# Performance work log

Hardware: AMD Instinct MI355X
Metric: run time of the kernel (lower is better)

Reference implementation:

```python
import jax, jax.numpy as jnp
import numpy as np

B, S, D, H = 4, 2048, 1024, 16
DK = D // H
THETA = 10000.0


def _rope(x, pos):
    # x: [..., s, d_k] interleaved-pair rotation (GPT-NeoX/torch-from-scratch style)
    half = DK // 2
    inv_freq = 1.0 / (THETA ** (jnp.arange(half, dtype=jnp.float32) * 2.0 / DK))
    ang = pos.astype(jnp.float32)[:, None] * inv_freq  # [s, half]
    cos, sin = jnp.cos(ang), jnp.sin(ang)
    x1, x2 = x[..., 0::2], x[..., 1::2]
    out = jnp.stack([x1 * cos - x2 * sin, x1 * sin + x2 * cos], axis=-1)
    return out.reshape(x.shape)


def setup_inputs() -> dict:
    key = jax.random.key(0)
    ks = jax.random.split(key, 5)
    w_scale = 1.0 / np.sqrt(D)
    return {
        "x": jax.random.normal(ks[0], (B, S, D), dtype=jnp.float32),
        "W_q": jax.random.normal(ks[1], (D, D), dtype=jnp.float32) * w_scale,
        "W_k": jax.random.normal(ks[2], (D, D), dtype=jnp.float32) * w_scale,
        "W_v": jax.random.normal(ks[3], (D, D), dtype=jnp.float32) * w_scale,
        "W_o": jax.random.normal(ks[4], (D, D), dtype=jnp.float32) * w_scale,
        "token_positions": jnp.arange(S, dtype=jnp.int32),
    }


def reference(x, W_q, W_k, W_v, W_o, token_positions):
    b, s, d = x.shape

    def proj(W):  # x @ W.T, split heads -> [b, h, s, d_k]
        y = jnp.einsum('bsd,ed->bse', x, W)
        return y.reshape(b, s, H, DK).transpose(0, 2, 1, 3)

    Q, K, V = proj(W_q), proj(W_k), proj(W_v)
    Q = _rope(Q, token_positions)
    K = _rope(K, token_positions)

    scores = jnp.einsum('bhqd,bhkd->bhqk', Q, K) / jnp.sqrt(jnp.float32(DK))
    causal = jnp.tril(jnp.ones((s, s), dtype=bool))
    scores = jnp.where(causal, scores, -jnp.inf)
    attn = jax.nn.softmax(scores, axis=-1)
    out = jnp.einsum('bhqk,bhkd->bhqd', attn, V)
    out = out.transpose(0, 2, 1, 3).reshape(b, s, d)
    return jnp.einsum('bsd,ed->bse', out, W_o)
```

## Files before the change

kernel.cpp:

```cpp
#include <hip/hip_runtime.h>
#include <stdint.h>

#define B_ 4
#define S_ 2048
#define D_ 1024
#define H_ 16
#define DK_ 64
#define M_ (B_*S_)

typedef __attribute__((ext_vector_type(8))) short short8;
typedef __attribute__((ext_vector_type(4))) float f32x4;
typedef __attribute__((ext_vector_type(16))) float f32x16;
typedef __attribute__((ext_vector_type(2))) unsigned int u32x2;

static __device__ __forceinline__ float bf2f(unsigned short s) {
  union { unsigned u; float f; } v; v.u = ((unsigned)s) << 16; return v.f;
}
static __device__ __forceinline__ unsigned short f2bf(float f) {
  union { float f; unsigned u; } v; v.f = f;
  unsigned r = v.u + 0x7fffu + ((v.u >> 16) & 1u);
  return (unsigned short)(r >> 16);
}
static __device__ __forceinline__ unsigned cvtpk_bf16(float lo, float hi) {
  unsigned r;
  asm("v_cvt_pk_bf16_f32 %0, %1, %2" : "=v"(r) : "v"(lo), "v"(hi));
  return r;
}

#define GLDS16(g, l) __builtin_amdgcn_global_load_lds( \
    (const __attribute__((address_space(1))) unsigned int*)(g), \
    (__attribute__((address_space(3))) unsigned int*)(l), 16, 0, 0)

__global__ void cvt_all_kernel(const float* __restrict__ x,
                               const float* __restrict__ w0, const float* __restrict__ w1,
                               const float* __restrict__ w2, const float* __restrict__ w3,
                               const int* __restrict__ pos,
                               unsigned short* __restrict__ xb,
                               unsigned short* __restrict__ o0, unsigned short* __restrict__ o1,
                               unsigned short* __restrict__ o2, unsigned short* __restrict__ o3,
                               float2* __restrict__ tab) {
  int idx = blockIdx.x * 256 + threadIdx.x;
  if (idx >= 3145728) {
    int tix = idx - 3145728;
    int s = tix >> 5, j = tix & 31;
    float freq = exp2f(-(float)j * (13.287712379549449f / 32.0f));
    float ang = (float)pos[s] * freq;
    float sn, cs;
    sincosf(ang, &sn, &cs);
    tab[tix] = make_float2(cs, sn);
    return;
  }
  const float* src; unsigned short* dst; int i;
  if (idx < 2097152) { src = x; dst = xb; i = idx; }
  else {
    int widx = idx - 2097152;
    int w = widx >> 18; i = widx & 262143;
    src = (w == 0) ? w0 : (w == 1) ? w1 : (w == 2) ? w2 : w3;
    dst = (w == 0) ? o0 : (w == 1) ? o1 : (w == 2) ? o2 : o3;
  }
  float4 v = ((const float4*)src)[i];
  ushort4 o;
  o.x = f2bf(v.x); o.y = f2bf(v.y); o.z = f2bf(v.z); o.w = f2bf(v.w);
  ((ushort4*)dst)[i] = o;
}

#define GEMM_BODY \
  __shared__ __align__(16) char lA[2][128*128]; \
  __shared__ __align__(16) char lB[2][128*128]; \
  int t = threadIdx.x; \
  int wave = t >> 6, lane = t & 63; \
  int ln15 = lane & 15, lgrp = lane >> 4; \
  int wr = wave >> 1, wc = wave & 1; \
  f32x4 acc[4][4]; \
  _Pragma("unroll") \
  for (int m = 0; m < 4; ++m) \
    _Pragma("unroll") \
    for (int n = 0; n < 4; ++n) { f32x4 z = {0.f,0.f,0.f,0.f}; acc[m][n] = z; } \
  const char* pA[4]; const char* pB[4]; int sdst[4]; \
  _Pragma("unroll") \
  for (int i_ = 0; i_ < 4; ++i_) { \
    int a_ = (i_*256 + t) << 4; \
    int r_ = a_ >> 7; \
    int cb_ = (a_ & 127) ^ ((r_ & 7) << 4); \
    sdst[i_] = a_; \
    pA[i_] = Ab + (size_t)r_*(K*2) + cb_; \
    pB[i_] = Bb + (size_t)r_*(K*2) + cb_; \
  } \
  GSTAGE(0); \
  __syncthreads(); \
  { int cur = 0; \
    for (int k0 = 0; k0 < K; k0 += 64) { \
      if (k0 + 64 < K) GSTAGE(cur ^ 1); \
      GEMM_COMPUTE(cur); \
      __syncthreads(); \
      cur ^= 1; \
    } }

#define GSTAGE(bufi) do { \
    _Pragma("unroll") \
    for (int i_ = 0; i_ < 4; ++i_) { \
      GLDS16(pA[i_], lA[bufi] + sdst[i_]); \
      GLDS16(pB[i_], lB[bufi] + sdst[i_]); \
      pA[i_] += 128; pB[i_] += 128; \
    } \
  } while (0)

#define GEMM_COMPUTE(bufi) do { \
    const char* cA_ = lA[bufi]; \
    const char* cB_ = lB[bufi]; \
    _Pragma("unroll") \
    for (int kf = 0; kf < 2; ++kf) { \
      int cb = kf*64 + lgrp*16; \
      short8 af[4], bfr[4]; \
      _Pragma("unroll") \
      for (int m = 0; m < 4; ++m) { \
        int r = wr*64 + m*16 + ln15; \
        af[m] = *(const short8*)(cA_ + r*128 + (cb ^ ((r & 7) << 4))); \
      } \
      _Pragma("unroll") \
      for (int n = 0; n < 4; ++n) { \
        int r = wc*64 + n*16 + ln15; \
        bfr[n] = *(const short8*)(cB_ + r*128 + (cb ^ ((r & 7) << 4))); \
      } \
      __builtin_amdgcn_s_setprio(1); \
      _Pragma("unroll") \
      for (int m = 0; m < 4; ++m) \
        _Pragma("unroll") \
        for (int n = 0; n < 4; ++n) \
          acc[m][n] = __builtin_amdgcn_mfma_f32_16x16x32_bf16(af[m], bfr[n], acc[m][n], 0, 0, 0); \
      __builtin_amdgcn_s_setprio(0); \
    } \
  } while (0)

__global__ __launch_bounds__(256) void gemm_qkv(const unsigned short* __restrict__ A,
                                                const unsigned short* __restrict__ W,
                                                const float2* __restrict__ Tab,
                                                unsigned short* __restrict__ Qo,
                                                unsigned short* __restrict__ Ko,
                                                unsigned short* __restrict__ Vo) {
  const int K = 1024;
  int bid = blockIdx.x;
  int wg = (bid & 7) * 192 + (bid >> 3);
  int bm = wg / 24, bn = wg % 24;
  const char* Ab = (const char*)A + (size_t)bm * 128 * (K*2);
  const char* Bb = (const char*)W + (size_t)bn * 128 * (K*2);
  GEMM_BODY

  if (bn < 16) {
    unsigned short* Out = (bn < 8) ? Qo : Ko;
    float qs = (bn < 8) ? (0.125f * 1.4426950408889634f) : 1.0f;
#pragma unroll
    for (int m = 0; m < 4; ++m)
#pragma unroll
      for (int n = 0; n < 4; ++n)
#pragma unroll
        for (int r = 0; r < 4; ++r) {
          int row = bm*128 + wr*64 + m*16 + lgrp*4 + r;
          int cc = (bn & 7)*128 + wc*64 + n*16 + ln15;
          int b = row >> 11, s = row & (S_-1);
          int h = cc >> 6, dk = cc & 63;
          float v = acc[m][n][r];
          float p = __shfl_xor(v, 1);
          float2 cssn = Tab[(s << 5) + (dk >> 1)];
          float sgn = (dk & 1) ? cssn.y : -cssn.y;
          float o = (v * cssn.x + p * sgn) * qs;
          Out[(((size_t)(b*H_ + h)*S_ + s) << 6) + dk] = f2bf(o);
        }
  } else {
#pragma unroll
    for (int m = 0; m < 4; ++m)
#pragma unroll
      for (int n = 0; n < 4; ++n)
#pragma unroll
        for (int r = 0; r < 4; ++r) {
          int row = bm*128 + wr*64 + m*16 + lgrp*4 + r;
          int cc = (bn - 16)*128 + wc*64 + n*16 + ln15;
          int b = row >> 11, s = row & (S_-1);
          int h = cc >> 6, dk = cc & 63;
          Vo[(((size_t)(b*H_ + h)*DK_ + dk) * S_) + s] = f2bf(acc[m][n][r]);
        }
  }
}

__global__ __launch_bounds__(256) void gemm_out(const unsigned short* __restrict__ A,
                                                const unsigned short* __restrict__ W,
                                                float* __restrict__ Out) {
  const int K = 1024, N = 1024;
  int bid = blockIdx.x;
  int wg = (bid & 7) * 64 + (bid >> 3);
  int bm = wg >> 3, bn = wg & 7;
  const char* Ab = (const char*)A + (size_t)bm * 128 * (K*2);
  const char* Bb = (const char*)W + (size_t)bn * 128 * (K*2);
  GEMM_BODY

#pragma unroll
  for (int m = 0; m < 4; ++m)
#pragma unroll
    for (int n = 0; n < 4; ++n)
#pragma unroll
      for (int r = 0; r < 4; ++r) {
        int row = bm*128 + wr*64 + m*16 + lgrp*4 + r;
        int col = bn*128 + wc*64 + n*16 + ln15;
        Out[(size_t)row * N + col] = acc[m][n][r];
      }
}

__global__ __launch_bounds__(512) void attn_kernel(const unsigned short* __restrict__ Q,
                                                   const unsigned short* __restrict__ Kg,
                                                   const unsigned short* __restrict__ VT,
                                                   unsigned short* __restrict__ O) {
  int bid = blockIdx.x;
  int bh = bid & 63;
  int grp = bid >> 6;
  int qt = (grp < 4) ? (7 - grp) : (grp - 4);
  int b = bh >> 4, h = bh & 15;
  const int qbase = qt * 256;
  const unsigned short* Qp = Q + (((size_t)bh * S_ + qbase) << 6);
  const char* Kp = (const char*)(Kg + ((size_t)bh * S_ << 6));
  const char* Vp = (const char*)(VT + (size_t)bh * DK_ * S_);

  __shared__ __align__(16) char lK[3][64*128];
  __shared__ __align__(16) char lV[3][64*128];

  int t = threadIdx.x, wave = t >> 6, lane = t & 63;
  int ln31 = lane & 31, hi = lane >> 5;
  int qw = wave * 32;
  int qg = qbase + qw + ln31;

  short8 qf[4];
#pragma unroll
  for (int kk = 0; kk < 4; ++kk)
    qf[kk] = *(const short8*)(Qp + (size_t)(qw + ln31)*64 + kk*16 + hi*8);

  f32x16 oc[2];
#pragma unroll
  for (int dh = 0; dh < 2; ++dh)
#pragma unroll
    for (int r = 0; r < 16; ++r) oc[dh][r] = 0.f;
  float li = 0.f;

  const int nt = 4*qt + 4;

  int a0 = t << 4;
  int r0 = a0 >> 7;
  int cb0 = (a0 & 127) ^ ((r0 & 7) << 4);
  int kdst = a0;
  const char* pK = Kp + (size_t)r0*128 + cb0;
  const char* pV = Vp + (size_t)r0*(S_*2) + cb0;
#define STAGE_KV(kbuf, vbuf) do { \
    GLDS16(pK, (kbuf) + kdst); \
    GLDS16(pV, (vbuf) + kdst); \
    pK += 64*128; pV += 128; \
  } while (0)

  char *Ka = lK[0], *Kb_ = lK[1], *Kc = lK[2];
  char *Va = lV[0], *Vb = lV[1], *Vc = lV[2];

  STAGE_KV(Ka, Va);
  STAGE_KV(Kb_, Vb);
  asm volatile("s_waitcnt vmcnt(2)" ::: "memory");
  __builtin_amdgcn_s_barrier();

  for (int kt = 0; kt < nt; ++kt) {
    bool more = (kt + 2 < nt);
    if (more) STAGE_KV(Kc, Vc);

    const char* cK = Ka;
    const char* cV = Va;
    bool active = (kt*64 <= qbase + qw + 31);
    bool diag   = (kt*64 + 63 > qbase + qw);

    if (active) {
      f32x16 sc[2];
      __builtin_amdgcn_s_setprio(1);
#pragma unroll
      for (int t2 = 0; t2 < 2; ++t2) {
        f32x16 a;
#pragma unroll
        for (int r = 0; r < 16; ++r) a[r] = 0.f;
        int rK = t2*32 + ln31;
        int swz = (rK & 7) << 4;
#pragma unroll
        for (int kk = 0; kk < 4; ++kk) {
          short8 kfr = *(const short8*)(cK + rK*128 + ((kk*32 + hi*16) ^ swz));
          a = __builtin_amdgcn_mfma_f32_32x32x16_bf16(kfr, qf[kk], a, 0, 0, 0);
        }
        sc[t2] = a;
      }
      __builtin_amdgcn_s_setprio(0);

      if (diag) {
#pragma unroll
        for (int t2 = 0; t2 < 2; ++t2)
#pragma unroll
          for (int r = 0; r < 16; ++r) {
            int kv = kt*64 + t2*32 + (r & 3) + 8*(r >> 2) + 4*hi;
            if (kv > qg) sc[t2][r] = -__builtin_inff();
          }
      }

      float lss[4] = {0.f, 0.f, 0.f, 0.f};
#pragma unroll
      for (int t2 = 0; t2 < 2; ++t2)
#pragma unroll
        for (int r = 0; r < 16; ++r) {
          float pv = __builtin_amdgcn_exp2f(sc[t2][r]);
          sc[t2][r] = pv; lss[r & 3] += pv;
        }
      li += (lss[0] + lss[1]) + (lss[2] + lss[3]);

#pragma unroll
      for (int kk = 0; kk < 4; ++kk) {
        int base = 8*(kk & 1), tt = kk >> 1;
        unsigned P0 = cvtpk_bf16(sc[tt][base+0], sc[tt][base+1]);
        unsigned P1 = cvtpk_bf16(sc[tt][base+2], sc[tt][base+3]);
        unsigned Q0 = cvtpk_bf16(sc[tt][base+4], sc[tt][base+5]);
        unsigned Q1 = cvtpk_bf16(sc[tt][base+6], sc[tt][base+7]);
        u32x2 r01 = __builtin_amdgcn_permlane32_swap(P0, Q0, false, false);
        u32x2 s01 = __builtin_amdgcn_permlane32_swap(P1, Q1, false, false);
        union { unsigned u[4]; short8 s8; } pf;
        pf.u[0] = r01[0]; pf.u[1] = s01[0]; pf.u[2] = r01[1]; pf.u[3] = s01[1];
        __builtin_amdgcn_s_setprio(1);
#pragma unroll
        for (int dh = 0; dh < 2; ++dh) {
          int rV = dh*32 + ln31;
          short8 vfr = *(const short8*)(cV + rV*128 + (((kk*32 + hi*16)) ^ ((rV & 7) << 4)));
          oc[dh] = __builtin_amdgcn_mfma_f32_32x32x16_bf16(vfr, pf.s8, oc[dh], 0, 0, 0);
        }
        __builtin_amdgcn_s_setprio(0);
      }
    }

    if (more) asm volatile("s_waitcnt vmcnt(2)" ::: "memory");
    else      asm volatile("s_waitcnt vmcnt(0)" ::: "memory");
    __builtin_amdgcn_s_barrier();

    char* tk = Ka; Ka = Kb_; Kb_ = Kc; Kc = tk;
    char* tv = Va; Va = Vb;  Vb = Vc;  Vc = tv;
  }
#undef STAGE_KV

  float lf = li + __shfl_xor(li, 32);
  float rinv = 1.0f / lf;
#pragma unroll
  for (int dh = 0; dh < 2; ++dh)
#pragma unroll
    for (int rg = 0; rg < 4; ++rg) {
      ushort4 pk4;
      pk4.x = f2bf(oc[dh][rg*4+0] * rinv);
      pk4.y = f2bf(oc[dh][rg*4+1] * rinv);
      pk4.z = f2bf(oc[dh][rg*4+2] * rinv);
      pk4.w = f2bf(oc[dh][rg*4+3] * rinv);
      int dk = dh*32 + 8*rg + 4*hi;
      *(ushort4*)(O + (((size_t)(b*S_ + qg)) << 10) + h*64 + dk) = pk4;
    }
}

extern "C" void kernel_launch(void* const* d_in, const int* in_sizes, int n_in,
                              void* d_out, int out_size, void* d_ws, size_t ws_size,
                              hipStream_t stream) {
  const float* x  = (const float*)d_in[0];
  const float* Wq = (const float*)d_in[1];
  const float* Wk = (const float*)d_in[2];
  const float* Wv = (const float*)d_in[3];
  const float* Wo = (const float*)d_in[4];
  const int* pos  = (const int*)d_in[5];

  char* ws = (char*)d_ws;
  unsigned short* xb  = (unsigned short*)(ws + 0);
  unsigned short* wqb = (unsigned short*)(ws + 16777216);
  unsigned short* wkb = (unsigned short*)(ws + 18874368);
  unsigned short* wvb = (unsigned short*)(ws + 20971520);
  unsigned short* wob = (unsigned short*)(ws + 23068672);
  unsigned short* Qb  = (unsigned short*)(ws + 25165824);
  unsigned short* Kb  = (unsigned short*)(ws + 41943040);
  unsigned short* VTb = (unsigned short*)(ws + 58720256);
  float2* tab = (float2*)d_out;
  unsigned short* Ob  = xb;

  cvt_all_kernel<<<12544, 256, 0, stream>>>(x, Wq, Wk, Wv, Wo, pos,
                                            xb, wqb, wkb, wvb, wob, tab);

  gemm_qkv<<<1536, 256, 0, stream>>>(xb, wqb, tab, Qb, Kb, VTb);

  attn_kernel<<<512, 512, 0, stream>>>(Qb, Kb, VTb, Ob);

  gemm_out<<<512, 256, 0, stream>>>(Ob, wob, (float*)d_out);
}
```

Before: 147.8 us.

## Split QKV projection into 256x256 8-wave QK GEMM and separate V GEMM

Replaces the single 128x128-tile QKV GEMM with a dedicated Q/K GEMM that uses 256x256 tiles, 512 threads, and an 8-phase interleaved prefetch schedule with explicit vmcnt waits and barriers, plus the RoPE epilogue. V is computed by a separate 128x128 GEMM launch. Larger tiles are meant to raise arithmetic intensity and hide load latency through finer-grained staging. The cost is an extra kernel launch and only 256 blocks at one block per CU for the Q/K part, which may leave the device under-filled.

Result: no change. 149.9 us (+1.4%).

```diff
diff --git a/kernel.cpp b/kernel.cpp
--- a/kernel.cpp
+++ b/kernel.cpp
@@ -30,6 +30,9 @@
 #define GLDS16(g, l) __builtin_amdgcn_global_load_lds( \
     (const __attribute__((address_space(1))) unsigned int*)(g), \
     (__attribute__((address_space(3))) unsigned int*)(l), 16, 0, 0)
+
+#define CFENCE() asm volatile("" ::: "memory")
+#define BARRIER() do { CFENCE(); __builtin_amdgcn_s_barrier(); CFENCE(); } while (0)
 
 __global__ void cvt_all_kernel(const float* __restrict__ x,
                                const float* __restrict__ w0, const float* __restrict__ w1,
@@ -64,6 +67,140 @@
   ((ushort4*)dst)[i] = o;
 }
 
+__global__ __launch_bounds__(512, 1) void gemm_qk8(const unsigned short* __restrict__ A,
+                                                   const unsigned short* __restrict__ W,
+                                                   const float2* __restrict__ Tab,
+                                                   unsigned short* __restrict__ Qo,
+                                                   unsigned short* __restrict__ Ko) {
+  __shared__ __align__(16) char lA[2*2*16384];
+  __shared__ __align__(16) char lB[2*2*16384];
+
+  int bid = blockIdx.x;
+  int wg = (bid & 7) * 32 + (bid >> 3);
+  int bm = wg >> 3, bn = wg & 7;
+
+  int t = threadIdx.x;
+  int wave = t >> 6, lane = t & 63;
+  int ln15 = lane & 15, lgrp = lane >> 4;
+  int wr = wave >> 2, wc = wave & 3;
+
+  const char* Ab = (const char*)A + (size_t)bm * 256 * 2048;
+  const char* Bb = (const char*)W + (size_t)bn * 256 * 2048;
+
+  int r0 = t >> 3;
+  int u0 = ((t << 4) & 127) ^ ((r0 & 7) << 4);
+  int d0 = t << 4;
+
+#define STG_A(sl, hf, kt) do { \
+    const char* g_ = Ab + (size_t)((hf)*128 + r0)*2048 + (size_t)(kt)*128 + u0; \
+    GLDS16(g_,            lA + (sl)*32768 + (hf)*16384 + d0); \
+    GLDS16(g_ + 64*2048,  lA + (sl)*32768 + (hf)*16384 + d0 + 8192); \
+  } while (0)
+#define STG_B(sl, hf, kt) do { \
+    const char* g_ = Bb + (size_t)((hf)*128 + r0)*2048 + (size_t)(kt)*128 + u0; \
+    GLDS16(g_,            lB + (sl)*32768 + (hf)*16384 + d0); \
+    GLDS16(g_ + 64*2048,  lB + (sl)*32768 + (hf)*16384 + d0 + 8192); \
+  } while (0)
+
+  f32x4 acc[8][4];
+#pragma unroll
+  for (int m = 0; m < 8; ++m)
+#pragma unroll
+    for (int n = 0; n < 4; ++n) { f32x4 z = {0.f,0.f,0.f,0.f}; acc[m][n] = z; }
+
+  const char* lAh = lA + wr * 16384;
+  const char* lBh = lB + (wc >> 1) * 16384;
+  int rB0 = (wc & 1) * 64 + ln15;
+  int kb = lgrp * 16;
+  int swz = (ln15 & 7) << 4;
+
+  short8 bfr[4][2];
+
+#define PHASE(sl, q, STAGES) do { \
+    short8 af0[2], af1[2]; \
+    if ((q) == 0) { \
+      _Pragma("unroll") \
+      for (int n = 0; n < 4; ++n) \
+        _Pragma("unroll") \
+        for (int ks = 0; ks < 2; ++ks) \
+          bfr[n][ks] = *(const short8*)(lBh + (sl)*32768 + (rB0 + n*16)*128 + ((ks*64 + kb) ^ swz)); \
+    } \
+    _Pragma("unroll") \
+    for (int ks = 0; ks < 2; ++ks) { \
+      af0[ks] = *(const short8*)(lAh + (sl)*32768 + ((2*(q))*16 + ln15)*128 + ((ks*64 + kb) ^ swz)); \
+      af1[ks] = *(const short8*)(lAh + (sl)*32768 + ((2*(q)+1)*16 + ln15)*128 + ((ks*64 + kb) ^ swz)); \
+    } \
+    STAGES; \
+    BARRIER(); \
+    __builtin_amdgcn_s_setprio(1); \
+    _Pragma("unroll") \
+    for (int n = 0; n < 4; ++n) \
+      _Pragma("unroll") \
+      for (int ks = 0; ks < 2; ++ks) { \
+        acc[2*(q)][n]   = __builtin_amdgcn_mfma_f32_16x16x32_bf16(af0[ks], bfr[n][ks], acc[2*(q)][n], 0, 0, 0); \
+        acc[2*(q)+1][n] = __builtin_amdgcn_mfma_f32_16x16x32_bf16(af1[ks], bfr[n][ks], acc[2*(q)+1][n], 0, 0, 0); \
+      } \
+    __builtin_amdgcn_s_setprio(0); \
+  } while (0)
+
+  STG_B(0, 0, 0); STG_B(0, 1, 0);
+  STG_A(0, 0, 0); STG_A(0, 1, 0);
+  STG_B(1, 0, 1); STG_B(1, 1, 1);
+  asm volatile("s_waitcnt vmcnt(0)" ::: "memory");
+  __builtin_amdgcn_s_barrier();
+  CFENCE();
+
+  for (int i = 0; i < 8; ++i) {
+    bool more = (i < 7);
+    int k1 = 2*i + 1, k2 = 2*i + 2, k3 = 2*i + 3;
+
+    PHASE(0, 0, { STG_A(1, 0, k1); });
+    BARRIER();
+    PHASE(0, 1, { STG_A(1, 1, k1); });
+    BARRIER();
+    PHASE(0, 2, { if (more) STG_B(0, 0, k2); });
+    BARRIER();
+    PHASE(0, 3, { if (more) STG_B(0, 1, k2); });
+    if (more) asm volatile("s_waitcnt vmcnt(4)" ::: "memory");
+    else      asm volatile("s_waitcnt vmcnt(0)" ::: "memory");
+    BARRIER();
+    PHASE(1, 0, { if (more) STG_A(0, 0, k2); });
+    BARRIER();
+    PHASE(1, 1, { if (more) STG_A(0, 1, k2); });
+    BARRIER();
+    PHASE(1, 2, { if (more) STG_B(1, 0, k3); });
+    BARRIER();
+    PHASE(1, 3, { if (more) STG_B(1, 1, k3); });
+    if (more) asm volatile("s_waitcnt vmcnt(4)" ::: "memory");
+    else      asm volatile("s_waitcnt vmcnt(0)" ::: "memory");
+    BARRIER();
+  }
+#undef PHASE
+#undef STG_A
+#undef STG_B
+
+#pragma unroll
+  for (int m = 0; m < 8; ++m)
+#pragma unroll
+    for (int n = 0; n < 4; ++n)
+#pragma unroll
+      for (int rr = 0; rr < 4; ++rr) {
+        int row = bm*256 + wr*128 + m*16 + lgrp*4 + rr;
+        int col = bn*256 + wc*64 + n*16 + ln15;
+        unsigned short* Out = (col < 1024) ? Qo : Ko;
+        float qs = (col < 1024) ? (0.125f * 1.4426950408889634f) : 1.0f;
+        int cc = col & 1023;
+        int b = row >> 11, s = row & (S_-1);
+        int h = cc >> 6, dk = cc & 63;
+        float v = acc[m][n][rr];
+        float p = __shfl_xor(v, 1);
+        float2 cssn = Tab[(s << 5) + (dk >> 1)];
+        float sgn = (dk & 1) ? cssn.y : -cssn.y;
+        float o = (v * cssn.x + p * sgn) * qs;
+        Out[(((size_t)(b*H_ + h)*S_ + s) << 6) + dk] = f2bf(o);
+      }
+}
+
 #define GEMM_BODY \
   __shared__ __align__(16) char lA[2][128*128]; \
   __shared__ __align__(16) char lB[2][128*128]; \
@@ -132,54 +269,29 @@
     } \
   } while (0)
 
-__global__ __launch_bounds__(256) void gemm_qkv(const unsigned short* __restrict__ A,
-                                                const unsigned short* __restrict__ W,
-                                                const float2* __restrict__ Tab,
-                                                unsigned short* __restrict__ Qo,
-                                                unsigned short* __restrict__ Ko,
-                                                unsigned short* __restrict__ Vo) {
+__global__ __launch_bounds__(256) void gemm_v(const unsigned short* __restrict__ A,
+                                              const unsigned short* __restrict__ W,
+                                              unsigned short* __restrict__ Vo) {
   const int K = 1024;
   int bid = blockIdx.x;
-  int wg = (bid & 7) * 192 + (bid >> 3);
-  int bm = wg / 24, bn = wg % 24;
+  int wg = (bid & 7) * 64 + (bid >> 3);
+  int bm = wg >> 3, bn = wg & 7;
   const char* Ab = (const char*)A + (size_t)bm * 128 * (K*2);
   const char* Bb = (const char*)W + (size_t)bn * 128 * (K*2);
   GEMM_BODY
 
-  if (bn < 16) {
-    unsigned short* Out = (bn < 8) ? Qo : Ko;
-    float qs = (bn < 8) ? (0.125f * 1.4426950408889634f) : 1.0f;
-#pragma unroll
-    for (int m = 0; m < 4; ++m)
-#pragma unroll
-      for (int n = 0; n < 4; ++n)
-#pragma unroll
-        for (int r = 0; r < 4; ++r) {
-          int row = bm*128 + wr*64 + m*16 + lgrp*4 + r;
-          int cc = (bn & 7)*128 + wc*64 + n*16 + ln15;
-          int b = row >> 11, s = row & (S_-1);
-          int h = cc >> 6, dk = cc & 63;
-          float v = acc[m][n][r];
-          float p = __shfl_xor(v, 1);
-          float2 cssn = Tab[(s << 5) + (dk >> 1)];
-          float sgn = (dk & 1) ? cssn.y : -cssn.y;
-          float o = (v * cssn.x + p * sgn) * qs;
-          Out[(((size_t)(b*H_ + h)*S_ + s) << 6) + dk] = f2bf(o);
-        }
-  } else {
-#pragma unroll
-    for (int m = 0; m < 4; ++m)
-#pragma unroll
-      for (int n = 0; n < 4; ++n)
-#pragma unroll
-        for (int r = 0; r < 4; ++r) {
-          int row = bm*128 + wr*64 + m*16 + lgrp*4 + r;
-          int cc = (bn - 16)*128 + wc*64 + n*16 + ln15;
-          int b = row >> 11, s = row & (S_-1);
-          int h = cc >> 6, dk = cc & 63;
-          Vo[(((size_t)(b*H_ + h)*DK_ + dk) * S_) + s] = f2bf(acc[m][n][r]);
-        }
-  }
+#pragma unroll
+  for (int m = 0; m < 4; ++m)
+#pragma unroll
+    for (int n = 0; n < 4; ++n)
+#pragma unroll
+      for (int r = 0; r < 4; ++r) {
+        int row = bm*128 + wr*64 + m*16 + lgrp*4 + r;
+        int cc = bn*128 + wc*64 + n*16 + ln15;
+        int b = row >> 11, s = row & (S_-1);
+        int h = cc >> 6, dk = cc & 63;
+        Vo[(((size_t)(b*H_ + h)*DK_ + dk) * S_) + s] = f2bf(acc[m][n][r]);
+      }
 }
 
 __global__ __launch_bounds__(256) void gemm_out(const unsigned short* __restrict__ A,
@@ -381,7 +493,8 @@
   cvt_all_kernel<<<12544, 256, 0, stream>>>(x, Wq, Wk, Wv, Wo, pos,
                                             xb, wqb, wkb, wvb, wob, tab);
 
-  gemm_qkv<<<1536, 256, 0, stream>>>(xb, wqb, tab, Qb, Kb, VTb);
+  gemm_qk8<<<256, 512, 0, stream>>>(xb, wqb, tab, Qb, Kb);
+  gemm_v<<<512, 256, 0, stream>>>(xb, wvb, VTb);
 
   attn_kernel<<<512, 512, 0, stream>>>(Qb, Kb, VTb, Ob);
 
```
